# Performance work log

Hardware: AMD Instinct MI355X
Metric: run time of the kernel (lower is better)

Reference implementation:

```python
import jax, jax.numpy as jnp
import numpy as np

LN_EPS = 1e-5


def setup_inputs() -> dict:
    key = jax.random.key(0)
    k1, k2 = jax.random.split(key, 2)
    B, C, D, H, W = 2, 96, 32, 128, 128
    out_dim = 2 * C
    x = jax.random.normal(k1, (B, C, D, H, W), dtype=jnp.float32)
    # nn.Linear(8*C, out_dim, bias=False): weight shape (out_dim, 8*C)
    w = jax.random.normal(k2, (out_dim, 8 * C), dtype=jnp.float32) * 0.02
    gamma = jnp.ones((8 * C,), dtype=jnp.float32)
    beta = jnp.zeros((8 * C,), dtype=jnp.float32)
    return {"x": x, "w": w, "gamma": gamma, "beta": beta}


def reference(x, w, gamma, beta):
    B, C, D, H, W = x.shape
    D2, H2, W2 = D // 2, H // 2, W // 2
    # Strided 2x2x2 gather: reshape then move (dd,hh,ww) offsets next to C.
    # torch.cat order [x0..x7] = (dd,hh,ww) lexicographic, dd most significant,
    # with C channels per block -> layout (..., dd, hh, ww, C) flattened.
    xr = x.reshape(B, C, D2, 2, H2, 2, W2, 2)
    xr = xr.transpose(0, 2, 4, 6, 3, 5, 7, 1)  # (B, D2, H2, W2, dd, hh, ww, C)
    xf = xr.reshape(B, D2, H2, W2, 8 * C)
    # LayerNorm over last dim
    mu = jnp.mean(xf, axis=-1, keepdims=True)
    xc = xf - mu
    var = jnp.mean(xc * xc, axis=-1, keepdims=True)
    xn = xc * jax.lax.rsqrt(var + LN_EPS) * gamma + beta
    # Linear (no bias): y = xn @ w.T
    y = jnp.einsum('bdhwc,oc->bdhwo', xn, w)
    # back to channels-first (B, out_dim, D2, H2, W2)
    return y.transpose(0, 4, 1, 2, 3)
```

## Files before the change

### kernel.cpp

```cpp
#include <hip/hip_runtime.h>
#include <hip/hip_bf16.h>

typedef __attribute__((ext_vector_type(8))) short short8;
typedef __attribute__((ext_vector_type(4))) float f32x4;

#define LN_EPS 1e-5f

__device__ __forceinline__ unsigned short f2bf(float f) {
  union { float f; unsigned u; } v; v.f = f;
  unsigned r = v.u + 0x7FFFu + ((v.u >> 16) & 1u);
  return (unsigned short)(r >> 16);
}

__device__ __forceinline__ unsigned cvt_pk_bf16(float a, float b) {
  unsigned r;
  asm("v_cvt_pk_bf16_f32 %0, %1, %2" : "=v"(r) : "v"(a), "v"(b));
  return r;
}

__device__ __forceinline__ int a_addr(int row, int colb) {
  return row * 1536 + (colb ^ ((row & 7) << 4));
}


__global__ __launch_bounds__(256) void pm_prep(
    const float* __restrict__ w, const float* __restrict__ g,
    const float* __restrict__ be, unsigned short* __restrict__ wg,
    float* __restrict__ sb) {
  const int o = blockIdx.x;
  const int t = threadIdx.x;
  const int lane = t & 63, wv = t >> 6;
  __shared__ float red[4][2];
  float sa = 0.f, ba = 0.f;
#pragma unroll
  for (int u = 0; u < 3; ++u) {
    int kp = t + 256 * u;
    int dh = kp / 192;
    int rem = kp - dh * 192;
    int c = rem >> 1, ww = rem & 1;
    int k = dh * 192 + ww * 96 + c;
    float wv_ = w[o * 768 + k];
    float v = wv_ * g[k];
    sa += v;
    ba += wv_ * be[k];
    int NT = o >> 4, ks = kp >> 5, qq = (kp >> 3) & 3, jj = kp & 7;
    wg[(((NT * 24 + ks) * 64) + qq * 16 + (o & 15)) * 8 + jj] = f2bf(v);
  }
#pragma unroll
  for (int d = 1; d < 64; d <<= 1) {
    sa += __shfl_xor(sa, d);
    ba += __shfl_xor(ba, d);
  }
  if (lane == 0) { red[wv][0] = sa; red[wv][1] = ba; }
  __syncthreads();
  if (t == 0) {
    sb[o] = red[0][0] + red[1][0] + red[2][0] + red[3][0];
    sb[192 + o] = red[0][1] + red[1][1] + red[2][1] + red[3][1];
  }
}

__global__ __launch_bounds__(256, 3) void pm_main(
    const float* __restrict__ x, const unsigned short* __restrict__ wg,
    const float* __restrict__ sb, float* __restrict__ out) {
  const int bid = blockIdx.x;
  const int wh = bid & 1;
  const int h2 = (bid >> 1) & 63;
  const int d2 = (bid >> 7) & 15;
  const int b = bid >> 11;
  const int t = threadIdx.x;
  const int lane = t & 63, wv = t >> 6;
  const int q = lane & 15, sc = lane >> 4;

  __shared__ __align__(16) unsigned char A_lds[32 * 1536];
  __shared__ float part[4][32][2];
  __shared__ float stats[32][2];

  const float* xb = x + (size_t)b * (96 * 32 * 128 * 128);
  const int cp0 = wv * 12 + sc * 3;
  const float* pc[3];
#pragma unroll
  for (int i = 0; i < 3; ++i)
    pc[i] = xb + (size_t)(2 * (cp0 + i)) * 524288 + wh * 64 + 4 * q;

  float sum0 = 0.f, sq0 = 0.f, sum1 = 0.f, sq1 = 0.f;
  float4 xa[3], xc[3];

  auto issue = [&](int p) {
    int off = (2 * d2 + (p >> 1)) * 16384 + (2 * h2 + (p & 1)) * 128;
#pragma unroll
    for (int i = 0; i < 3; ++i) {
      xa[i] = *(const float4*)(pc[i] + off);
      xc[i] = *(const float4*)(pc[i] + 524288 + off);
    }
  };

  auto consume = [&](int p) {
#pragma unroll
    for (int i = 0; i < 3; ++i) {
      float4 f0 = xa[i], f1 = xc[i];
      sum0 += (f0.x + f0.y) + (f1.x + f1.y);
      sq0  += f0.x * f0.x + f0.y * f0.y + f1.x * f1.x + f1.y * f1.y;
      sum1 += (f0.z + f0.w) + (f1.z + f1.w);
      sq1  += f0.z * f0.z + f0.w * f0.w + f1.z * f1.z + f1.w * f1.w;
      int colb = p * 384 + 8 * (cp0 + i);
      uint2 v0, v1;
      v0.x = cvt_pk_bf16(f0.x, f0.y); v0.y = cvt_pk_bf16(f1.x, f1.y);
      v1.x = cvt_pk_bf16(f0.z, f0.w); v1.y = cvt_pk_bf16(f1.z, f1.w);
      *(uint2*)&A_lds[a_addr(2 * q, colb)] = v0;
      *(uint2*)&A_lds[a_addr(2 * q + 1, colb)] = v1;
    }
  };

  const int al = lane & 15, ah = lane >> 4;
  const short8* wgs = (const short8*)wg;
  f32x4 acc[2][3];
#pragma unroll
  for (int mt = 0; mt < 2; ++mt)
#pragma unroll
    for (int nt = 0; nt < 3; ++nt) acc[mt][nt] = {0.f, 0.f, 0.f, 0.f};

  issue(0);

#pragma unroll
  for (int p = 0; p < 4; ++p) {
    consume(p);
    if (p == 3) {
      sum0 += __shfl_xor(sum0, 16); sum0 += __shfl_xor(sum0, 32);
      sq0  += __shfl_xor(sq0, 16);  sq0  += __shfl_xor(sq0, 32);
      sum1 += __shfl_xor(sum1, 16); sum1 += __shfl_xor(sum1, 32);
      sq1  += __shfl_xor(sq1, 16);  sq1  += __shfl_xor(sq1, 32);
      if (sc == 0) {
        part[wv][2 * q][0] = sum0;     part[wv][2 * q][1] = sq0;
        part[wv][2 * q + 1][0] = sum1; part[wv][2 * q + 1][1] = sq1;
      }
    }
    __syncthreads();

    short8 bfr[6][3];
#pragma unroll
    for (int ksi = 0; ksi < 6; ++ksi)
#pragma unroll
      for (int nt = 0; nt < 3; ++nt)
        bfr[ksi][nt] = wgs[((wv * 3 + nt) * 24 + (p * 6 + ksi)) * 64 + lane];

    if (p < 3) issue(p + 1);

    if (p == 3) {
      int row = t & 31;
      float S = part[0][row][0] + part[1][row][0] + part[2][row][0] + part[3][row][0];
      float Q = part[0][row][1] + part[1][row][1] + part[2][row][1] + part[3][row][1];
      float mu = S * (1.f / 768.f);
      float var = Q * (1.f / 768.f) - mu * mu;
      float rs = rsqrtf(var + LN_EPS);
      stats[row][0] = rs;
      stats[row][1] = mu * rs;
    }

#pragma unroll
    for (int ksi = 0; ksi < 6; ++ksi) {
      int ks = p * 6 + ksi;
      short8 afr[2];
#pragma unroll
      for (int mt = 0; mt < 2; ++mt)
        afr[mt] = *(const short8*)&A_lds[a_addr(mt * 16 + al, ks * 64 + ah * 16)];
#pragma unroll
      for (int nt = 0; nt < 3; ++nt)
#pragma unroll
        for (int mt = 0; mt < 2; ++mt)
          acc[mt][nt] = __builtin_amdgcn_mfma_f32_16x16x32_bf16(afr[mt], bfr[ksi][nt], acc[mt][nt], 0, 0, 0);
    }
  }
  __syncthreads();

#pragma unroll
  for (int nt = 0; nt < 3; ++nt) {
    int o = wv * 48 + nt * 16 + al;
    float Sv = sb[o], Bv = sb[192 + o];
    float* ob = out + (((size_t)(b * 192 + o) * 16 + d2) * 64 + h2) * 64 + wh * 32;
#pragma unroll
    for (int mt = 0; mt < 2; ++mt) {
      int m0 = mt * 16 + ah * 4;
      float4 y;
      y.x = stats[m0 + 0][0] * acc[mt][nt][0] - stats[m0 + 0][1] * Sv + Bv;
      y.y = stats[m0 + 1][0] * acc[mt][nt][1] - stats[m0 + 1][1] * Sv + Bv;
      y.z = stats[m0 + 2][0] * acc[mt][nt][2] - stats[m0 + 2][1] * Sv + Bv;
      y.w = stats[m0 + 3][0] * acc[mt][nt][3] - stats[m0 + 3][1] * Sv + Bv;
      *(float4*)(ob + m0) = y;
    }
  }
}

extern "C" void kernel_launch(void* const* d_in, const int* in_sizes, int n_in,
                              void* d_out, int out_size, void* d_ws, size_t ws_size,
                              hipStream_t stream) {
  (void)in_sizes; (void)n_in; (void)out_size; (void)ws_size;
  const float* x  = (const float*)d_in[0];
  const float* w  = (const float*)d_in[1];
  const float* g  = (const float*)d_in[2];
  const float* be = (const float*)d_in[3];
  unsigned short* wg = (unsigned short*)d_ws;
  float* sb = (float*)((char*)d_ws + 192 * 768 * sizeof(unsigned short));
  pm_prep<<<192, 256, 0, stream>>>(w, g, be, wg, sb);
  pm_main<<<4096, 256, 0, stream>>>(x, wg, sb, (float*)d_out);
}
```

Baseline: 156.5 us.

## Stream fp32 input directly to LDS and fuse LN stats into fragment build

Input tiles are now loaded with global_load_lds straight into a double-buffered fp32 LDS staging area, instead of being staged through registers and written back as swizzled bf16. Each wave then reads fp32 pairs from LDS, converts them to bf16 MFMA fragments on the fly, and accumulates the LayerNorm sum and sum-of-squares while doing so. Stats are reduced with shuffles, so the separate partial-sum LDS array and its cross-wave combine are gone. The aim is more load/compute overlap and lower register pressure. In exchange, every wave redoes the bf16 conversion and stats for the whole tile, LDS read traffic doubles because the data is fp32, and correctness depends on async LDS loads having completed before the barrier.

```diff
diff --git a/kernel.cpp b/kernel.cpp
--- a/kernel.cpp
+++ b/kernel.cpp
@@ -3,6 +3,7 @@
 
 typedef __attribute__((ext_vector_type(8))) short short8;
 typedef __attribute__((ext_vector_type(4))) float f32x4;
+typedef __attribute__((ext_vector_type(4))) unsigned uint4v;
 
 #define LN_EPS 1e-5f
 
@@ -16,10 +17,6 @@
   unsigned r;
   asm("v_cvt_pk_bf16_f32 %0, %1, %2" : "=v"(r) : "v"(a), "v"(b));
   return r;
-}
-
-__device__ __forceinline__ int a_addr(int row, int colb) {
-  return row * 1536 + (colb ^ ((row & 7) << 4));
 }
 
 
@@ -69,72 +66,43 @@
   const int b = bid >> 11;
   const int t = threadIdx.x;
   const int lane = t & 63, wv = t >> 6;
-  const int q = lane & 15, sc = lane >> 4;
+  const int al = lane & 15, ah = lane >> 4;
 
-  __shared__ __align__(16) unsigned char A_lds[32 * 1536];
-  __shared__ float part[4][32][2];
+  __shared__ __align__(16) float Af32[2][6144];
   __shared__ float stats[32][2];
 
-  const float* xb = x + (size_t)b * (96 * 32 * 128 * 128);
-  const int cp0 = wv * 12 + sc * 3;
-  const float* pc[3];
-#pragma unroll
-  for (int i = 0; i < 3; ++i)
-    pc[i] = xb + (size_t)(2 * (cp0 + i)) * 524288 + wh * 64 + 4 * q;
-
-  float sum0 = 0.f, sq0 = 0.f, sum1 = 0.f, sq1 = 0.f;
-  float4 xa[3], xc[3];
+  const float* xb = x + (size_t)b * 50331648 + wh * 64 + (lane & 15) * 4;
+  const int coff = lane >> 4;
 
   auto issue = [&](int p) {
-    int off = (2 * d2 + (p >> 1)) * 16384 + (2 * h2 + (p & 1)) * 128;
+    const int slot = p & 1;
+    const int off = (2 * d2 + (p >> 1)) * 16384 + (2 * h2 + (p & 1)) * 128;
 #pragma unroll
-    for (int i = 0; i < 3; ++i) {
-      xa[i] = *(const float4*)(pc[i] + off);
-      xc[i] = *(const float4*)(pc[i] + 524288 + off);
+    for (int i = 0; i < 6; ++i) {
+      const int c0 = wv * 24 + i * 4;
+      const float* g = xb + (size_t)(c0 + coff) * 524288 + off;
+      __builtin_amdgcn_global_load_lds(
+          (const __attribute__((address_space(1))) unsigned int*)g,
+          (__attribute__((address_space(3))) unsigned int*)&Af32[slot][c0 * 64],
+          16, 0, 0);
     }
   };
 
-  auto consume = [&](int p) {
-#pragma unroll
-    for (int i = 0; i < 3; ++i) {
-      float4 f0 = xa[i], f1 = xc[i];
-      sum0 += (f0.x + f0.y) + (f1.x + f1.y);
-      sq0  += f0.x * f0.x + f0.y * f0.y + f1.x * f1.x + f1.y * f1.y;
-      sum1 += (f0.z + f0.w) + (f1.z + f1.w);
-      sq1  += f0.z * f0.z + f0.w * f0.w + f1.z * f1.z + f1.w * f1.w;
-      int colb = p * 384 + 8 * (cp0 + i);
-      uint2 v0, v1;
-      v0.x = cvt_pk_bf16(f0.x, f0.y); v0.y = cvt_pk_bf16(f1.x, f1.y);
-      v1.x = cvt_pk_bf16(f0.z, f0.w); v1.y = cvt_pk_bf16(f1.z, f1.w);
-      *(uint2*)&A_lds[a_addr(2 * q, colb)] = v0;
-      *(uint2*)&A_lds[a_addr(2 * q + 1, colb)] = v1;
-    }
-  };
-
-  const int al = lane & 15, ah = lane >> 4;
-  const short8* wgs = (const short8*)wg;
+  float sumr[2] = {0.f, 0.f}, sqr[2] = {0.f, 0.f};
   f32x4 acc[2][3];
 #pragma unroll
   for (int mt = 0; mt < 2; ++mt)
 #pragma unroll
     for (int nt = 0; nt < 3; ++nt) acc[mt][nt] = {0.f, 0.f, 0.f, 0.f};
 
+  const short8* wgs = (const short8*)wg;
+
   issue(0);
 
 #pragma unroll
   for (int p = 0; p < 4; ++p) {
-    consume(p);
-    if (p == 3) {
-      sum0 += __shfl_xor(sum0, 16); sum0 += __shfl_xor(sum0, 32);
-      sq0  += __shfl_xor(sq0, 16);  sq0  += __shfl_xor(sq0, 32);
-      sum1 += __shfl_xor(sum1, 16); sum1 += __shfl_xor(sum1, 32);
-      sq1  += __shfl_xor(sq1, 16);  sq1  += __shfl_xor(sq1, 32);
-      if (sc == 0) {
-        part[wv][2 * q][0] = sum0;     part[wv][2 * q][1] = sq0;
-        part[wv][2 * q + 1][0] = sum1; part[wv][2 * q + 1][1] = sq1;
-      }
-    }
     __syncthreads();
+    if (p < 3) issue(p + 1);
 
     short8 bfr[6][3];
 #pragma unroll
@@ -143,31 +111,48 @@
       for (int nt = 0; nt < 3; ++nt)
         bfr[ksi][nt] = wgs[((wv * 3 + nt) * 24 + (p * 6 + ksi)) * 64 + lane];
 
-    if (p < 3) issue(p + 1);
-
-    if (p == 3) {
-      int row = t & 31;
-      float S = part[0][row][0] + part[1][row][0] + part[2][row][0] + part[3][row][0];
-      float Q = part[0][row][1] + part[1][row][1] + part[2][row][1] + part[3][row][1];
-      float mu = S * (1.f / 768.f);
-      float var = Q * (1.f / 768.f) - mu * mu;
-      float rs = rsqrtf(var + LN_EPS);
-      stats[row][0] = rs;
-      stats[row][1] = mu * rs;
-    }
-
+    const float* As = Af32[p & 1];
 #pragma unroll
     for (int ksi = 0; ksi < 6; ++ksi) {
-      int ks = p * 6 + ksi;
       short8 afr[2];
 #pragma unroll
-      for (int mt = 0; mt < 2; ++mt)
-        afr[mt] = *(const short8*)&A_lds[a_addr(mt * 16 + al, ks * 64 + ah * 16)];
+      for (int mt = 0; mt < 2; ++mt) {
+        const int base = (ksi * 16 + ah * 4) * 64 + (mt * 16 + al) * 2;
+        float2 e0 = *(const float2*)&As[base];
+        float2 e1 = *(const float2*)&As[base + 64];
+        float2 e2 = *(const float2*)&As[base + 128];
+        float2 e3 = *(const float2*)&As[base + 192];
+        sumr[mt] += ((e0.x + e0.y) + (e1.x + e1.y)) + ((e2.x + e2.y) + (e3.x + e3.y));
+        sqr[mt] += e0.x * e0.x + e0.y * e0.y + e1.x * e1.x + e1.y * e1.y
+                 + e2.x * e2.x + e2.y * e2.y + e3.x * e3.x + e3.y * e3.y;
+        uint4v u;
+        u.x = cvt_pk_bf16(e0.x, e0.y);
+        u.y = cvt_pk_bf16(e1.x, e1.y);
+        u.z = cvt_pk_bf16(e2.x, e2.y);
+        u.w = cvt_pk_bf16(e3.x, e3.y);
+        afr[mt] = __builtin_bit_cast(short8, u);
+      }
 #pragma unroll
       for (int nt = 0; nt < 3; ++nt)
 #pragma unroll
         for (int mt = 0; mt < 2; ++mt)
           acc[mt][nt] = __builtin_amdgcn_mfma_f32_16x16x32_bf16(afr[mt], bfr[ksi][nt], acc[mt][nt], 0, 0, 0);
+    }
+  }
+
+#pragma unroll
+  for (int mt = 0; mt < 2; ++mt) {
+    sumr[mt] += __shfl_xor(sumr[mt], 16); sumr[mt] += __shfl_xor(sumr[mt], 32);
+    sqr[mt]  += __shfl_xor(sqr[mt], 16);  sqr[mt]  += __shfl_xor(sqr[mt], 32);
+  }
+  if (lane < 16) {
+#pragma unroll
+    for (int mt = 0; mt < 2; ++mt) {
+      float mu = sumr[mt] * (1.f / 768.f);
+      float var = sqr[mt] * (1.f / 768.f) - mu * mu;
+      float rs = rsqrtf(var + LN_EPS);
+      stats[mt * 16 + al][0] = rs;
+      stats[mt * 16 + al][1] = mu * rs;
     }
   }
   __syncthreads();
```

After: 171.8 us. +9.7%, slower.
